# Kernel optimization log

Measured on AMD Instinct MI355X. Metric: run time of the kernel, lower is better.

## Reference

```python
import jax, jax.numpy as jnp
import numpy as np

B, S, D = 2, 512, 2048          # batch, seq, hidden
H, Dh = 16, 128                 # heads, head_dim
E, K, G, TG = 8, 2, 2, 1        # experts, top_k, n_group, topk_group
I, IS = 1024, 1024              # routed / shared expert intermediate
ROUTED_SCALE = 2.5
EPS = 1e-6
ROPE_THETA = 10000.0


def setup_inputs() -> dict:
    key = jax.random.key(0)
    ks = jax.random.split(key, 13)
    p = lambda k, shape, s=0.02: jax.random.normal(k, shape, jnp.float32) * s
    return {
        "hidden_states": jax.random.normal(ks[0], (B, S, D), jnp.float32),
        "ln1_w": jnp.ones((D,), jnp.float32),
        "ln2_w": jnp.ones((D,), jnp.float32),
        "wq": p(ks[1], (D, H * Dh)),
        "wk": p(ks[2], (D, H * Dh)),
        "wv": p(ks[3], (D, H * Dh)),
        "wo": p(ks[4], (H * Dh, D)),
        "gate_w": p(ks[5], (E, D)),
        "gate_bias": p(ks[6], (E,), 0.1),
        "w_gate": p(ks[7], (E, D, I)),
        "w_up": p(ks[8], (E, D, I)),
        "w_down": p(ks[9], (E, I, D)),
        "sw_gate": p(ks[10], (D, IS)),
        "sw_up": p(ks[11], (D, IS)),
        "sw_down": p(ks[12], (IS, D)),
    }


def _rmsnorm(x, w):
    var = jnp.mean(x * x, axis=-1, keepdims=True)
    return x * jax.lax.rsqrt(var + EPS) * w


def _rope_cos_sin(seq_len):
    inv_freq = 1.0 / (ROPE_THETA ** (jnp.arange(0, Dh, 2, dtype=jnp.float32) / Dh))
    ang = jnp.arange(seq_len, dtype=jnp.float32)[:, None] * inv_freq  # [S, Dh/2]
    return jnp.cos(ang)[None, :, None, :], jnp.sin(ang)[None, :, None, :]


def _apply_rope(x, cos, sin):
    x1, x2 = jnp.split(x, 2, axis=-1)
    return jnp.concatenate([x1 * cos - x2 * sin, x2 * cos + x1 * sin], axis=-1)


def _attention(x, wq, wk, wv, wo):
    q = (x @ wq).reshape(B, S, H, Dh)
    k = (x @ wk).reshape(B, S, H, Dh)
    v = (x @ wv).reshape(B, S, H, Dh)
    cos, sin = _rope_cos_sin(S)
    q = _apply_rope(q, cos, sin)
    k = _apply_rope(k, cos, sin)
    scores = jnp.einsum('bqhd,bkhd->bhqk', q, k) * (1.0 / np.sqrt(Dh).astype(np.float32))
    causal = jnp.tril(jnp.ones((S, S), bool))
    scores = jnp.where(causal, scores, jnp.finfo(scores.dtype).min)
    attn = jax.nn.softmax(scores, axis=-1)
    out = jnp.einsum('bhqk,bkhd->bqhd', attn, v).reshape(B, S, H * Dh)
    return out @ wo


def _moe(x, gate_w, gate_bias, w_gate, w_up, w_down, sw_gate, sw_up, sw_down):
    # x: [T, D]. noaux_tc grouped top-k routing (DeepSeek-V3 style).
    T = x.shape[0]
    logits = x @ gate_w.T                      # [T, E]
    scores = jax.nn.sigmoid(logits)
    sc = scores + gate_bias                    # selection scores with correction bias
    grp = sc.reshape(T, G, E // G)
    group_scores = jnp.sum(jax.lax.top_k(grp, 2)[0], axis=-1)  # top-2 sum per group [T,G]
    _, gidx = jax.lax.top_k(group_scores, TG)
    gmask = jnp.zeros((T, G), bool).at[jnp.arange(T)[:, None], gidx].set(True)
    emask = jnp.broadcast_to(gmask[:, :, None], (T, G, E // G)).reshape(T, E)
    masked = jnp.where(emask, sc, -jnp.inf)
    _, idx = jax.lax.top_k(masked, K)          # [T, K] expert ids
    w = jnp.take_along_axis(scores, idx, axis=-1)
    w = w / jnp.sum(w, axis=-1, keepdims=True)  # norm_topk_prob=True
    # dense combine weights [T, E] (zero except K entries per token)
    cw = jnp.zeros((T, E), x.dtype).at[jnp.arange(T)[:, None], idx].add(w)

    def body(acc, xs):
        wg, wu, wd, cwe = xs
        y = (jax.nn.silu(x @ wg) * (x @ wu)) @ wd  # SiluAndMul gated MLP
        return acc + cwe[:, None] * y, None

    routed, _ = jax.lax.scan(body, jnp.zeros_like(x), (w_gate, w_up, w_down, cw.T))
    shared = (jax.nn.silu(x @ sw_gate) * (x @ sw_up)) @ sw_down
    return routed * ROUTED_SCALE + shared


def reference(hidden_states, ln1_w, ln2_w, wq, wk, wv, wo, gate_w, gate_bias,
              w_gate, w_up, w_down, sw_gate, sw_up, sw_down):
    h = hidden_states
    h = h + _attention(_rmsnorm(h, ln1_w), wq, wk, wv, wo)
    x = _rmsnorm(h, ln2_w).reshape(B * S, D)
    moe_out = _moe(x, gate_w, gate_bias, w_gate, w_up, w_down,
                   sw_gate, sw_up, sw_down).reshape(B, S, D)
    return h + moe_out
```

## Files before the change

### kernel.cpp

```cpp
#include <hip/hip_runtime.h>

typedef __bf16 bf16x4 __attribute__((ext_vector_type(4)));
typedef __bf16 bf16x8 __attribute__((ext_vector_type(8)));
typedef _Float16 f16x4 __attribute__((ext_vector_type(4)));
typedef _Float16 f16x8 __attribute__((ext_vector_type(8)));
typedef float  f32x4  __attribute__((ext_vector_type(4)));

#define THREADS 256
constexpr int BK = 32, BKP = 40;

constexpr size_t MB = 1024*1024;
constexpr size_t oH2    = 0;
constexpr size_t oXB2   = 8*MB;
constexpr size_t oRT    = 12*MB;
constexpr size_t oWQKVT = 16*MB;
constexpr size_t oWOT   = 64*MB;
constexpr size_t oXN1   = 80*MB;
constexpr size_t oQKV   = 88*MB;
constexpr size_t oSCF   = 112*MB;
constexpr size_t oQKS   = 144*MB;
constexpr size_t oQKSL  = 152*MB;
constexpr size_t oVT    = 16*MB;
constexpr size_t oVTL   = 20*MB;
constexpr size_t oATT   = 24*MB;
constexpr size_t oPB    = 40*MB;
constexpr size_t oPBL2  = 88*MB;
constexpr size_t oWGUT  = 16*MB;
constexpr size_t oWDT   = 80*MB;
constexpr size_t oSGUT  = 112*MB;
constexpr size_t oSDT   = 120*MB;
constexpr size_t oHB    = 140*MB;
constexpr size_t oY     = 144*MB;
constexpr size_t oSHB   = 24*MB;
constexpr size_t oSDB   = 26*MB;
constexpr size_t oEIDX = oRT;
constexpr size_t oEW   = oRT + 8192;
constexpr size_t oSLOT = oRT + 16384;
constexpr size_t oLIST = oRT + 24576;
constexpr size_t oCNT  = oRT + 32768;
constexpr size_t oOFF  = oRT + 33024;
constexpr size_t oCUR  = oRT + 33280;

__device__ __forceinline__ bf16x8 bzero8() {
  bf16x8 z;
#pragma unroll
  for (int j = 0; j < 8; ++j) z[j] = (__bf16)0.f;
  return z;
}

template<int OM>
__global__ void transpose_kernel(const float* __restrict__ in, __bf16* __restrict__ out,
                                 int ldin, int ldout, int zlo,
                                 long inBH, long inBL, long outB, long plane) {
  __shared__ float tile[64][65];
  int z = blockIdx.z;
  const float* inp = in + (long)(z / zlo) * inBH + (long)(z % zlo) * inBL;
  __bf16* outp = out + (long)z * outB;
  int r0 = blockIdx.y * 64, c0 = blockIdx.x * 64;
  int tid = threadIdx.x;
#pragma unroll
  for (int i = 0; i < 4; ++i) {
    int lin = tid + i * 256;
    int r = lin >> 4, c4 = (lin & 15) << 2;
    f32x4 v = *(const f32x4*)(inp + (long)(r0 + r) * ldin + c0 + c4);
    tile[r][c4] = v[0]; tile[r][c4+1] = v[1]; tile[r][c4+2] = v[2]; tile[r][c4+3] = v[3];
  }
  __syncthreads();
#pragma unroll
  for (int i = 0; i < 4; ++i) {
    int lin = tid + i * 256;
    int oR = lin >> 4, oC4 = (lin & 15) << 2;
    __bf16* dst = outp + (long)(c0 + oR) * ldout + r0 + oC4;
    if constexpr (OM == 3) {
      f16x4 hv;
#pragma unroll
      for (int j = 0; j < 4; ++j) hv[j] = (_Float16)tile[oC4 + j][oR];
      *reinterpret_cast<f16x4*>(dst) = hv;
    } else {
      bf16x4 hi, lo;
#pragma unroll
      for (int j = 0; j < 4; ++j) {
        float v = tile[oC4 + j][oR];
        hi[j] = (__bf16)v;
        if constexpr (OM == 2) lo[j] = (__bf16)(v - (float)hi[j]);
      }
      *(bf16x4*)dst = hi;
      if constexpr (OM == 2) *(bf16x4*)(dst + plane) = lo;
    }
  }
}

template<int MODE, int SP, bool RESID, bool CAUSAL, bool KTRI, int TBM = 128, int TBN = 128>
__global__ __launch_bounds__(256, 2)
void gemm_kernel(const void* __restrict__ Av, const void* __restrict__ Bv, float* __restrict__ C,
                 const float* __restrict__ Rres,
                 int M, int N, int K, int lda, int ldb, int ldc,
                 int zlo, long aHi, long aLo, long bHi, long bLo, long cHi, long cLo,
                 long aPlane, long bPlane,
                 const int* __restrict__ counts, const int* __restrict__ offsets,
                 const int* __restrict__ gather) {
  const int n0 = blockIdx.x * TBN;
  const int m0 = blockIdx.y * TBM;
  const int z  = blockIdx.z;
  if (CAUSAL && n0 > m0) return;

  const float*  Af = (const float*)Av;
  const __bf16* Ah = (const __bf16*)Av;
  const __bf16* Bh = (const __bf16*)Bv;

  int mcount; int rowbase = 0;
  long aoff = 0, boff = 0, coff = 0;
  if constexpr (MODE == 0) {
    mcount = M;
    int zh = z / zlo, zl = z % zlo;
    aoff = (long)zh*aHi + (long)zl*aLo;
    boff = (long)zh*bHi + (long)zl*bLo;
    coff = (long)zh*cHi + (long)zl*cLo;
  } else {
    mcount = counts[z];
    rowbase = offsets[z];
    if (m0 >= mcount) return;
    boff = (long)z*bHi;
  }

  constexpr bool TRI  = (SP == 1 || SP == 2);
  constexpr bool F16  = (SP == 3 || SP == 4);
  constexpr bool AFLY = (SP == 1 || SP == 4);
  constexpr int ABUF = TBM*BKP;
  constexpr int BBUF = TBN*BKP;
  constexpr int WTM = TBM/2, WTN = TBN/2;
  constexpr int MI = WTM/16, MJ = WTN/16;
  __shared__ __align__(16) __bf16 As[(TRI?2:1)*ABUF];
  __shared__ __align__(16) __bf16 Bs[(TRI?2:1)*BBUF];

  const int tid = threadIdx.x;
  const int lane = tid & 63, wave = tid >> 6;
  const int wm = wave >> 1, wn = wave & 1;
  const int lq = lane >> 4, lr = lane & 15;

  int kend = K;
  if (KTRI) { int ke = m0 + TBM; kend = ke < K ? ke : K; }

  f32x4 acc[MI][MJ] = {};

  constexpr int NAF = AFLY ? TBM/32 : 1;
  constexpr int NAH = (!AFLY) ? TBM/64 : 1;
  constexpr int NB  = TBN/64;
  f32x4  arf[NAF];
  bf16x8 arh[NAH], arl[NAH];
  bf16x8 brh[NB],  brl[NB];

  auto loadAB = [&](int kk) {
    if constexpr (AFLY) {
#pragma unroll
      for (int it = 0; it < NAF; ++it) {
        int lin = tid + it*THREADS;
        int row = lin >> 3, c4 = (lin & 7) << 2;
        int gr = m0 + row;
        f32x4 zv; zv[0]=0.f; zv[1]=0.f; zv[2]=0.f; zv[3]=0.f;
        arf[it] = (gr < mcount) ? *(const f32x4*)(Af + aoff + (long)gr*lda + kk + c4) : zv;
      }
    } else {
#pragma unroll
      for (int it = 0; it < NAH; ++it) {
        int lin = tid + it*THREADS;
        int row = lin >> 2, c8 = (lin & 3) << 3;
        int gr = m0 + row;
        arh[it] = bzero8();
        if constexpr (SP == 2) arl[it] = bzero8();
        if (gr < mcount) {
          long arow;
          if constexpr (MODE == 1) arow = gather[rowbase + gr];
          else if constexpr (MODE == 2) arow = rowbase + gr;
          else arow = gr;
          const __bf16* p = Ah + aoff + arow*(long)lda + kk + c8;
          arh[it] = *(const bf16x8*)p;
          if constexpr (SP == 2) arl[it] = *(const bf16x8*)(p + aPlane);
        }
      }
    }
#pragma unroll
    for (int it = 0; it < NB; ++it) {
      int lin = tid + it*THREADS;
      int row = lin >> 2, c8 = (lin & 3) << 3;
      const __bf16* p = Bh + boff + (long)(n0+row)*ldb + kk + c8;
      brh[it] = *(const bf16x8*)p;
      if constexpr (TRI) brl[it] = *(const bf16x8*)(p + bPlane);
    }
  };

  auto writeAB = [&]() {
    if constexpr (AFLY) {
#pragma unroll
      for (int it = 0; it < NAF; ++it) {
        int lin = tid + it*THREADS;
        int row = lin >> 3, c4 = (lin & 7) << 2;
        if constexpr (SP == 4) {
          f16x4 hv;
#pragma unroll
          for (int j = 0; j < 4; ++j) hv[j] = (_Float16)arf[it][j];
          *reinterpret_cast<f16x4*>(As + row*BKP + c4) = hv;
        } else {
          bf16x4 hi, lo;
#pragma unroll
          for (int j = 0; j < 4; ++j) {
            hi[j] = (__bf16)arf[it][j];
            lo[j] = (__bf16)(arf[it][j] - (float)hi[j]);
          }
          *(bf16x4*)(As + row*BKP + c4) = hi;
          *(bf16x4*)(As + ABUF + row*BKP + c4) = lo;
        }
      }
    } else {
#pragma unroll
      for (int it = 0; it < NAH; ++it) {
        int lin = tid + it*THREADS;
        int row = lin >> 2, c8 = (lin & 3) << 3;
        *(bf16x8*)(As + row*BKP + c8) = arh[it];
        if constexpr (SP == 2) *(bf16x8*)(As + ABUF + row*BKP + c8) = arl[it];
      }
    }
#pragma unroll
    for (int it = 0; it < NB; ++it) {
      int lin = tid + it*THREADS;
      int row = lin >> 2, c8 = (lin & 3) << 3;
      *(bf16x8*)(Bs + row*BKP + c8) = brh[it];
      if constexpr (TRI) *(bf16x8*)(Bs + BBUF + row*BKP + c8) = brl[it];
    }
  };

  loadAB(0);
  writeAB();
  __syncthreads();

  for (int k0 = 0; k0 < kend; k0 += BK) {
    const bool hn = (k0 + BK < kend);
    if (hn) loadAB(k0 + BK);

    const __bf16* ap = As + (wm*WTM + lr)*BKP + lq*8;
    const __bf16* bp = Bs + (wn*WTN + lr)*BKP + lq*8;
    if constexpr (F16) {
      f16x8 fa[MI];
#pragma unroll
      for (int i = 0; i < MI; ++i)
        fa[i] = *reinterpret_cast<const f16x8*>(ap + i*16*BKP);
#pragma unroll
      for (int j = 0; j < MJ; ++j) {
        f16x8 fb = *reinterpret_cast<const f16x8*>(bp + j*16*BKP);
#pragma unroll
        for (int i = 0; i < MI; ++i)
          acc[i][j] = __builtin_amdgcn_mfma_f32_16x16x32_f16(fa[i], fb, acc[i][j], 0, 0, 0);
      }
    } else {
      bf16x8 fa[MI], fal[MI];
#pragma unroll
      for (int i = 0; i < MI; ++i) {
        fa[i] = *(const bf16x8*)(ap + i*16*BKP);
        if constexpr (TRI) fal[i] = *(const bf16x8*)(ap + ABUF + i*16*BKP);
      }
#pragma unroll
      for (int j = 0; j < MJ; ++j) {
        bf16x8 fb = *(const bf16x8*)(bp + j*16*BKP);
        if constexpr (TRI) {
          bf16x8 fbl = *(const bf16x8*)(bp + BBUF + j*16*BKP);
#pragma unroll
          for (int i = 0; i < MI; ++i) {
            acc[i][j] = __builtin_amdgcn_mfma_f32_16x16x32_bf16(fa[i],  fbl, acc[i][j], 0, 0, 0);
            acc[i][j] = __builtin_amdgcn_mfma_f32_16x16x32_bf16(fal[i], fb,  acc[i][j], 0, 0, 0);
            acc[i][j] = __builtin_amdgcn_mfma_f32_16x16x32_bf16(fa[i],  fb,  acc[i][j], 0, 0, 0);
          }
        } else {
#pragma unroll
          for (int i = 0; i < MI; ++i)
            acc[i][j] = __builtin_amdgcn_mfma_f32_16x16x32_bf16(fa[i], fb, acc[i][j], 0, 0, 0);
        }
      }
    }

    if (hn) {
      __syncthreads();
      writeAB();
      __syncthreads();
    }
  }

#pragma unroll
  for (int i = 0; i < MI; ++i) {
#pragma unroll
    for (int rg = 0; rg < 4; ++rg) {
      int lrow = wm*WTM + i*16 + lq*4 + rg;
      int gr = m0 + lrow;
      if (gr < mcount) {
        long crow = coff + (long)(rowbase + gr)*ldc;
#pragma unroll
        for (int j = 0; j < MJ; ++j) {
          int col = n0 + wn*WTN + j*16 + lr;
          float val = acc[i][j][rg];
          if constexpr (RESID) val += Rres[(long)gr*ldc + col];
          C[crow + col] = val;
        }
      }
    }
  }
}

template<int MODE>
__global__ __launch_bounds__(256, 2)
void gugemm_kernel(const __bf16* __restrict__ A, const __bf16* __restrict__ B,
                   __bf16* __restrict__ O, int M, int K, int lda, int ldb, long bHi,
                   const int* __restrict__ counts, const int* __restrict__ offsets,
                   const int* __restrict__ gather) {
  const int n0 = blockIdx.x * 64;
  const int m0 = blockIdx.y * 64;
  const int z  = blockIdx.z;

  int mcount; int rowbase = 0; long boff = 0;
  if constexpr (MODE == 1) {
    mcount = counts[z];
    rowbase = offsets[z];
    if (m0 >= mcount) return;
    boff = (long)z*bHi;
  } else {
    mcount = M;
  }

  constexpr int TBUF = 64*BKP;
  __shared__ __align__(16) __bf16 As[TBUF];
  __shared__ __align__(16) __bf16 Bg[TBUF];
  __shared__ __align__(16) __bf16 Bu[TBUF];

  const int tid = threadIdx.x;
  const int lane = tid & 63, wave = tid >> 6;
  const int wm = wave >> 1, wn = wave & 1;
  const int lq = lane >> 4, lr = lane & 15;

  f32x4 accG[2][2] = {}, accU[2][2] = {};

  bf16x8 ar, bg, bu;
  const int srow = tid >> 2, sc8 = (tid & 3) << 3;
  long aBase; bool aOK;
  {
    int gr = m0 + srow;
    aOK = gr < mcount;
    long arow = 0;
    if (aOK) {
      if constexpr (MODE == 1) arow = gather[rowbase + gr];
      else arow = gr;
    }
    aBase = arow*(long)lda;
  }
  const long gBase = boff + (long)(n0 + srow)*ldb;
  const long uBase = boff + (long)(1024 + n0 + srow)*ldb;

  auto loadAB = [&](int kk) {
    ar = aOK ? *(const bf16x8*)(A + aBase + kk + sc8) : bzero8();
    bg = *(const bf16x8*)(B + gBase + kk + sc8);
    bu = *(const bf16x8*)(B + uBase + kk + sc8);
  };
  auto writeAB = [&]() {
    *(bf16x8*)(As + srow*BKP + sc8) = ar;
    *(bf16x8*)(Bg + srow*BKP + sc8) = bg;
    *(bf16x8*)(Bu + srow*BKP + sc8) = bu;
  };

  loadAB(0);
  writeAB();
  __syncthreads();

  for (int k0 = 0; k0 < K; k0 += BK) {
    const bool hn = (k0 + BK < K);
    if (hn) loadAB(k0 + BK);

    const __bf16* ap  = As + (wm*32 + lr)*BKP + lq*8;
    const __bf16* bgp = Bg + (wn*32 + lr)*BKP + lq*8;
    const __bf16* bup = Bu + (wn*32 + lr)*BKP + lq*8;
    bf16x8 fa[2];
    fa[0] = *(const bf16x8*)(ap);
    fa[1] = *(const bf16x8*)(ap + 16*BKP);
#pragma unroll
    for (int j = 0; j < 2; ++j) {
      bf16x8 fg = *(const bf16x8*)(bgp + j*16*BKP);
      bf16x8 fu = *(const bf16x8*)(bup + j*16*BKP);
#pragma unroll
      for (int i = 0; i < 2; ++i) {
        accG[i][j] = __builtin_amdgcn_mfma_f32_16x16x32_bf16(fa[i], fg, accG[i][j], 0, 0, 0);
        accU[i][j] = __builtin_amdgcn_mfma_f32_16x16x32_bf16(fa[i], fu, accU[i][j], 0, 0, 0);
      }
    }

    if (hn) {
      __syncthreads();
      writeAB();
      __syncthreads();
    }
  }

#pragma unroll
  for (int i = 0; i < 2; ++i) {
#pragma unroll
    for (int rg = 0; rg < 4; ++rg) {
      int lrow = wm*32 + i*16 + lq*4 + rg;
      int gr = m0 + lrow;
      if (gr < mcount) {
        long orow = (long)(rowbase + gr)*1024;
#pragma unroll
        for (int j = 0; j < 2; ++j) {
          int col = n0 + wn*32 + j*16 + lr;
          float g = accG[i][j][rg], u = accU[i][j][rg];
          float val = (g / (1.f + expf(-g))) * u;
          O[orow + col] = (__bf16)val;
        }
      }
    }
  }
}

template<int OM>
__global__ void rmsnorm_kernel(const float* __restrict__ x, const float* __restrict__ w,
                               __bf16* __restrict__ out, long plane) {
  const int row = blockIdx.x;
  const float* xr = x + (long)row * 2048;
  float ss = 0.f;
  for (int d = threadIdx.x; d < 2048; d += 256) { float v = xr[d]; ss += v*v; }
  __shared__ float red[4];
  int lane = threadIdx.x & 63, wave = threadIdx.x >> 6;
#pragma unroll
  for (int off = 32; off; off >>= 1) ss += __shfl_down(ss, off, 64);
  if (lane == 0) red[wave] = ss;
  __syncthreads();
  float tot = red[0] + red[1] + red[2] + red[3];
  float rs = rsqrtf(tot * (1.f/2048.f) + 1e-6f);
  __bf16* orow = out + (long)row * 2048;
  for (int d = threadIdx.x; d < 2048; d += 256) {
    float v = xr[d]*rs*w[d];
    if constexpr (OM == 3) {
      ((_Float16*)orow)[d] = (_Float16)v;
    } else {
      __bf16 h = (__bf16)v;
      orow[d] = h;
      if constexpr (OM == 2) orow[d + plane] = (__bf16)(v - (float)h);
    }
  }
}

__global__ void rope_split_kernel(const float* __restrict__ qkv, __bf16* __restrict__ o, long plane) {
  int tid = blockIdx.x*256 + threadIdx.x;
  int i = tid & 63;
  int th = tid >> 6;
  int h = th & 15;
  int t = th >> 4;
  int s = t & 511;
  long ib = (long)t*6144 + h*128;
  long ob = (long)t*4096 + h*128;
  float inv = 1.f / powf(10000.f, (float)i * (1.f/64.f));
  float ang = (float)s * inv;
  float c = cosf(ang), sn = sinf(ang);
  float q1 = qkv[ib+i], q2 = qkv[ib+64+i];
  float r1 = q1*c - q2*sn, r2 = q2*c + q1*sn;
  __bf16 h1 = (__bf16)r1, h2v = (__bf16)r2;
  o[ob+i] = h1;            o[ob+i+plane] = (__bf16)(r1 - (float)h1);
  o[ob+64+i] = h2v;        o[ob+64+i+plane] = (__bf16)(r2 - (float)h2v);
  float k1 = qkv[ib+2048+i], k2 = qkv[ib+2048+64+i];
  float s1 = k1*c - k2*sn, s2 = k2*c + k1*sn;
  __bf16 g1 = (__bf16)s1, g2 = (__bf16)s2;
  o[ob+2048+i] = g1;       o[ob+2048+i+plane] = (__bf16)(s1 - (float)g1);
  o[ob+2048+64+i] = g2;    o[ob+2048+64+i+plane] = (__bf16)(s2 - (float)g2);
}

__global__ void softmax_kernel(const float* __restrict__ sc, __bf16* __restrict__ p, long plane) {
  int r = blockIdx.x & 511;
  long bh = blockIdx.x >> 9;
  const float scale = 0.08838834764831845f;
  long base = (bh*512 + r)*512;
  int c0 = threadIdx.x, c1 = threadIdx.x + 256;
  float v0 = (c0 <= r) ? sc[base+c0]*scale : -3.0e38f;
  float v1 = (c1 <= r) ? sc[base+c1]*scale : -3.0e38f;
  float m = fmaxf(v0, v1);
  __shared__ float red[4];
  int lane = threadIdx.x & 63, wave = threadIdx.x >> 6;
#pragma unroll
  for (int off = 32; off; off >>= 1) m = fmaxf(m, __shfl_xor(m, off, 64));
  if (lane == 0) red[wave] = m;
  __syncthreads();
  m = fmaxf(fmaxf(red[0], red[1]), fmaxf(red[2], red[3]));
  __syncthreads();
  float e0 = (c0 <= r) ? expf(v0 - m) : 0.f;
  float e1 = (c1 <= r) ? expf(v1 - m) : 0.f;
  float s = e0 + e1;
#pragma unroll
  for (int off = 32; off; off >>= 1) s += __shfl_xor(s, off, 64);
  if (lane == 0) red[wave] = s;
  __syncthreads();
  s = red[0] + red[1] + red[2] + red[3];
  float inv = 1.f / s;
  float p0 = e0*inv, p1 = e1*inv;
  __bf16 h0 = (__bf16)p0, h1 = (__bf16)p1;
  p[base+c0] = h0; p[base+c0+plane] = (__bf16)(p0 - (float)h0);
  p[base+c1] = h1; p[base+c1+plane] = (__bf16)(p1 - (float)h1);
}

__global__ void zero8_kernel(int* c) { if (threadIdx.x < 8) c[threadIdx.x] = 0; }

__global__ void routing_kernel(const float* __restrict__ h2, const float* __restrict__ ln2w,
                               const float* __restrict__ gw, const float* __restrict__ gb,
                               __bf16* __restrict__ xb2,
                               int* __restrict__ eidx, float* __restrict__ ew,
                               int* __restrict__ counts) {
  int t = blockIdx.x;
  const float* xr = h2 + (long)t*2048;
  int lane = threadIdx.x & 63, wave = threadIdx.x >> 6;
  float ss = 0.f;
  for (int d = threadIdx.x; d < 2048; d += 256) { float v = xr[d]; ss += v*v; }
  __shared__ float red[4];
#pragma unroll
  for (int off = 32; off; off >>= 1) ss += __shfl_down(ss, off, 64);
  if (lane == 0) red[wave] = ss;
  __syncthreads();
  float rs = rsqrtf((red[0]+red[1]+red[2]+red[3]) * (1.f/2048.f) + 1e-6f);
  __bf16* xrow = xb2 + (long)t*2048;
  for (int d = threadIdx.x; d < 2048; d += 256) xrow[d] = (__bf16)(xr[d]*rs*ln2w[d]);
  __shared__ float lg[8];
  for (int e = wave; e < 8; e += 4) {
    const float* wr = gw + (long)e*2048;
    float acc = 0.f;
    for (int d = lane; d < 2048; d += 64) acc += (xr[d]*rs*ln2w[d]) * wr[d];
#pragma unroll
    for (int off = 32; off; off >>= 1) acc += __shfl_down(acc, off, 64);
    if (lane == 0) lg[e] = acc;
  }
  __syncthreads();
  if (threadIdx.x == 0) {
    float sg[8], sc[8];
#pragma unroll
    for (int e = 0; e < 8; ++e) { sg[e] = 1.f/(1.f+expf(-lg[e])); sc[e] = sg[e] + gb[e]; }
    float gs[2];
#pragma unroll
    for (int g = 0; g < 2; ++g) {
      float m1 = -3e38f, m2 = -3e38f;
#pragma unroll
      for (int j = 0; j < 4; ++j) {
        float v = sc[4*g+j];
        if (v > m1) { m2 = m1; m1 = v; } else if (v > m2) m2 = v;
      }
      gs[g] = m1 + m2;
    }
    int b4 = (gs[1] > gs[0]) ? 4 : 0;
    int i1 = 0; float v1 = -3e38f;
#pragma unroll
    for (int j = 0; j < 4; ++j) if (sc[b4+j] > v1) { v1 = sc[b4+j]; i1 = j; }
    int i2 = -1; float v2 = -3e38f;
#pragma unroll
    for (int j = 0; j < 4; ++j) if (j != i1 && sc[b4+j] > v2) { v2 = sc[b4+j]; i2 = j; }
    float w1 = sg[b4+i1], w2 = sg[b4+i2], s = w1 + w2;
    eidx[t*2] = b4+i1; eidx[t*2+1] = b4+i2;
    ew[t*2] = w1/s;    ew[t*2+1] = w2/s;
    atomicAdd(&counts[b4+i1], 1); atomicAdd(&counts[b4+i2], 1);
  }
}

__global__ void scan_kernel(const int* __restrict__ counts, int* __restrict__ offsets,
                            int* __restrict__ cursors) {
  if (threadIdx.x == 0 && blockIdx.x == 0) {
    int s = 0;
    for (int e = 0; e < 8; ++e) { offsets[e] = s; s += counts[e]; cursors[e] = 0; }
    offsets[8] = s;
  }
}

__global__ void scatter_kernel(const int* __restrict__ eidx, const int* __restrict__ offsets,
                               int* __restrict__ cursors, int* __restrict__ list,
                               int* __restrict__ slot) {
  int t = blockIdx.x*256 + threadIdx.x;
  if (t < 1024) {
#pragma unroll
    for (int kk = 0; kk < 2; ++kk) {
      int e = eidx[t*2+kk];
      int pos = atomicAdd(&cursors[e], 1);
      int g = offsets[e] + pos;
      list[g] = t;
      slot[t*2+kk] = g;
    }
  }
}

__global__ void combine_kernel(const float* __restrict__ h2, const float* __restrict__ y,
                               const float* __restrict__ sdown, const int* __restrict__ slot,
                               const float* __restrict__ ew, float* __restrict__ out) {
  int i = blockIdx.x*256 + threadIdx.x;
  int t = i >> 11;
  int d = i & 2047;
  float rv = ew[t*2]   * y[(long)slot[t*2]  *2048 + d]
           + ew[t*2+1] * y[(long)slot[t*2+1]*2048 + d];
  out[i] = h2[i] + sdown[i] + 2.5f * rv;
}

extern "C" void kernel_launch(void* const* d_in, const int* in_sizes, int n_in,
                              void* d_out, int out_size, void* d_ws, size_t ws_size,
                              hipStream_t stream) {
  const float* hid  = (const float*)d_in[0];
  const float* ln1  = (const float*)d_in[1];
  const float* ln2  = (const float*)d_in[2];
  const float* wq   = (const float*)d_in[3];
  const float* wk   = (const float*)d_in[4];
  const float* wv   = (const float*)d_in[5];
  const float* wo   = (const float*)d_in[6];
  const float* gw   = (const float*)d_in[7];
  const float* gb   = (const float*)d_in[8];
  const float* wgat = (const float*)d_in[9];
  const float* wup  = (const float*)d_in[10];
  const float* wdn  = (const float*)d_in[11];
  const float* swg  = (const float*)d_in[12];
  const float* swu  = (const float*)d_in[13];
  const float* swd  = (const float*)d_in[14];
  float* out = (float*)d_out;
  char* ws = (char*)d_ws;

  float*  h2    = (float*)(ws + oH2);
  __bf16* xb2   = (__bf16*)(ws + oXB2);
  __bf16* wqkvT = (__bf16*)(ws + oWQKVT);
  __bf16* woT   = (__bf16*)(ws + oWOT);
  __bf16* xn1   = (__bf16*)(ws + oXN1);
  float*  qkv   = (float*)(ws + oQKV);
  float*  scf   = (float*)(ws + oSCF);
  __bf16* qks   = (__bf16*)(ws + oQKS);
  __bf16* vtb   = (__bf16*)(ws + oVT);
  float*  att   = (float*)(ws + oATT);
  __bf16* pb    = (__bf16*)(ws + oPB);
  __bf16* wgut  = (__bf16*)(ws + oWGUT);
  __bf16* wdt   = (__bf16*)(ws + oWDT);
  __bf16* sgut  = (__bf16*)(ws + oSGUT);
  __bf16* sdt   = (__bf16*)(ws + oSDT);
  __bf16* hb    = (__bf16*)(ws + oHB);
  float*  ybuf  = (float*)(ws + oY);
  __bf16* shb   = (__bf16*)(ws + oSHB);
  float*  sdb   = (float*)(ws + oSDB);
  int*   eidx = (int*)(ws + oEIDX);
  float* ew   = (float*)(ws + oEW);
  int*   slot = (int*)(ws + oSLOT);
  int*   list = (int*)(ws + oLIST);
  int*   cnt  = (int*)(ws + oCNT);
  int*   offs = (int*)(ws + oOFF);
  int*   curs = (int*)(ws + oCUR);

  const long S22 = (long)2048*2048, S21 = (long)2048*1024;
  const long pQKS  = (oQKSL - oQKS) / 2;
  const long pVT   = 2*MB;
  const long pPB   = (oPBL2 - oPB) / 2;

  transpose_kernel<3><<<dim3(32,32,1), 256, 0, stream>>>(wq, wqkvT,          2048, 2048, 1, 0, 0, 0, 0);
  transpose_kernel<3><<<dim3(32,32,1), 256, 0, stream>>>(wk, wqkvT + S22,    2048, 2048, 1, 0, 0, 0, 0);
  transpose_kernel<3><<<dim3(32,32,1), 256, 0, stream>>>(wv, wqkvT + 2*S22,  2048, 2048, 1, 0, 0, 0, 0);
  transpose_kernel<3><<<dim3(32,32,1), 256, 0, stream>>>(wo, woT,            2048, 2048, 1, 0, 0, 0, 0);

  rmsnorm_kernel<3><<<1024, 256, 0, stream>>>(hid, ln1, xn1, 0);

  gemm_kernel<0, 3, false, false, false, 64, 128><<<dim3(48,16,1), 256, 0, stream>>>(
      xn1, wqkvT, qkv, nullptr, 1024, 6144, 2048, 2048, 2048, 6144,
      1, 0, 0, 0, 0, 0, 0, 0, 0, nullptr, nullptr, nullptr);

  rope_split_kernel<<<4096, 256, 0, stream>>>(qkv, qks, pQKS);

  transpose_kernel<2><<<dim3(2,8,32), 256, 0, stream>>>(
      qkv + 4096, vtb, 6144, 512, 16, (long)512*6144, 128, (long)128*512, pVT);

  gemm_kernel<0, 2, false, true, false, 64, 64><<<dim3(8,8,32), 256, 0, stream>>>(
      qks, qks + 2048, scf, nullptr, 512, 512, 128, 4096, 4096, 512,
      16, (long)512*4096, 128, (long)512*4096, 128, (long)16*512*512, (long)512*512,
      pQKS, pQKS, nullptr, nullptr, nullptr);

  softmax_kernel<<<16384, 256, 0, stream>>>(scf, pb, pPB);

  gemm_kernel<0, 2, false, false, true, 64, 64><<<dim3(2,8,32), 256, 0, stream>>>(
      pb, vtb, att, nullptr, 512, 128, 512, 512, 512, 2048,
      16, (long)16*512*512, (long)512*512, (long)16*128*512, (long)128*512,
      (long)512*2048, 128, pPB, pVT, nullptr, nullptr, nullptr);

  gemm_kernel<0, 4, true, false, false, 64, 64><<<dim3(32,16,1), 256, 0, stream>>>(
      att, woT, h2, hid, 1024, 2048, 2048, 2048, 2048, 2048,
      1, 0, 0, 0, 0, 0, 0, 0, 0, nullptr, nullptr, nullptr);

  zero8_kernel<<<1, 64, 0, stream>>>(cnt);
  routing_kernel<<<1024, 256, 0, stream>>>(h2, ln2, gw, gb, xb2, eidx, ew, cnt);
  scan_kernel<<<1, 64, 0, stream>>>(cnt, offs, curs);
  scatter_kernel<<<4, 256, 0, stream>>>(eidx, offs, curs, list, slot);

  transpose_kernel<1><<<dim3(16,32,8), 256, 0, stream>>>(wgat, wgut,        1024, 2048, 1, S21, 0, S22, 0);
  transpose_kernel<1><<<dim3(16,32,8), 256, 0, stream>>>(wup,  wgut + S21,  1024, 2048, 1, S21, 0, S22, 0);
  transpose_kernel<1><<<dim3(32,16,8), 256, 0, stream>>>(wdn,  wdt,         2048, 1024, 1, S21, 0, S21, 0);
  transpose_kernel<1><<<dim3(16,32,1), 256, 0, stream>>>(swg,  sgut,        1024, 2048, 1, 0, 0, 0, 0);
  transpose_kernel<1><<<dim3(16,32,1), 256, 0, stream>>>(swu,  sgut + S21,  1024, 2048, 1, 0, 0, 0, 0);
  transpose_kernel<1><<<dim3(32,16,1), 256, 0, stream>>>(swd,  sdt,         2048, 1024, 1, 0, 0, 0, 0);

  gugemm_kernel<1><<<dim3(16,16,8), 256, 0, stream>>>(
      xb2, wgut, hb, 1024, 2048, 2048, 2048, S22, cnt, offs, list);
  gemm_kernel<2, 0, false, false, false, 64, 64><<<dim3(32,16,8), 256, 0, stream>>>(
      hb, wdt, ybuf, nullptr, 1024, 2048, 1024, 1024, 1024, 2048,
      1, 0, 0, S21, 0, 0, 0, 0, 0, cnt, offs, nullptr);

  gugemm_kernel<0><<<dim3(16,16,1), 256, 0, stream>>>(
      xb2, sgut, shb, 1024, 2048, 2048, 2048, 0, nullptr, nullptr, nullptr);
  gemm_kernel<0, 0, false, false, false, 64, 64><<<dim3(32,16,1), 256, 0, stream>>>(
      shb, sdt, sdb, nullptr, 1024, 2048, 1024, 1024, 1024, 2048,
      1, 0, 0, 0, 0, 0, 0, 0, 0, nullptr, nullptr, nullptr);

  combine_kernel<<<8192, 256, 0, stream>>>(h2, ybuf, sdb, slot, ew, out);
}
```

Baseline: 706.1 us.

## Merge shared expert into grouped MoE GEMMs as ninth expert, widen gugemm K tile

The shared expert becomes a ninth group (z=8) in the grouped gate/up and down GEMM launches. Its weights are laid out contiguously after the routed experts, and counts[8]=1024 is set in the scan kernel. This removes two separate kernel launches and lets the shared-expert work fill the same grid as the routed experts. The gate/up kernel also moves from a K tile of 32 to 64, with two rows per thread per load, halving the number of barrier pairs per K sweep at the cost of more shared memory and registers. The combine kernel reads the shared output from rows 2048+ of the joint output buffer.

```diff
diff --git a/kernel.cpp b/kernel.cpp
--- a/kernel.cpp
+++ b/kernel.cpp
@@ -26,13 +26,11 @@
 constexpr size_t oPB    = 40*MB;
 constexpr size_t oPBL2  = 88*MB;
 constexpr size_t oWGUT  = 16*MB;
-constexpr size_t oWDT   = 80*MB;
-constexpr size_t oSGUT  = 112*MB;
+constexpr size_t oSGUT  = 80*MB;
+constexpr size_t oWDT   = 88*MB;
 constexpr size_t oSDT   = 120*MB;
-constexpr size_t oHB    = 140*MB;
-constexpr size_t oY     = 144*MB;
-constexpr size_t oSHB   = 24*MB;
-constexpr size_t oSDB   = 26*MB;
+constexpr size_t oHBC   = 124*MB;
+constexpr size_t oYC    = 130*MB;
 constexpr size_t oEIDX = oRT;
 constexpr size_t oEW   = oRT + 8192;
 constexpr size_t oSLOT = oRT + 16384;
@@ -304,27 +302,23 @@
   }
 }
 
-template<int MODE>
 __global__ __launch_bounds__(256, 2)
 void gugemm_kernel(const __bf16* __restrict__ A, const __bf16* __restrict__ B,
-                   __bf16* __restrict__ O, int M, int K, int lda, int ldb, long bHi,
+                   __bf16* __restrict__ O, int K, int lda, int ldb, long bHi,
                    const int* __restrict__ counts, const int* __restrict__ offsets,
                    const int* __restrict__ gather) {
+  constexpr int BKg = 64, BKP2 = 72;
   const int n0 = blockIdx.x * 64;
   const int m0 = blockIdx.y * 64;
   const int z  = blockIdx.z;
 
-  int mcount; int rowbase = 0; long boff = 0;
-  if constexpr (MODE == 1) {
-    mcount = counts[z];
-    rowbase = offsets[z];
-    if (m0 >= mcount) return;
-    boff = (long)z*bHi;
-  } else {
-    mcount = M;
-  }
-
-  constexpr int TBUF = 64*BKP;
+  const int mcount = counts[z];
+  const int rowbase = offsets[z];
+  if (m0 >= mcount) return;
+  const long boff = (long)z*bHi;
+  const bool shared = (z == 8);
+
+  constexpr int TBUF = 64*BKP2;
   __shared__ __align__(16) __bf16 As[TBUF];
   __shared__ __align__(16) __bf16 Bg[TBUF];
   __shared__ __align__(16) __bf16 Bu[TBUF];
@@ -336,55 +330,65 @@
 
   f32x4 accG[2][2] = {}, accU[2][2] = {};
 
-  bf16x8 ar, bg, bu;
-  const int srow = tid >> 2, sc8 = (tid & 3) << 3;
-  long aBase; bool aOK;
+  const int r0 = tid >> 3;
+  const int c8 = (tid & 7) << 3;
+  long aB0, aB1; bool aOK0, aOK1;
   {
-    int gr = m0 + srow;
-    aOK = gr < mcount;
-    long arow = 0;
-    if (aOK) {
-      if constexpr (MODE == 1) arow = gather[rowbase + gr];
-      else arow = gr;
-    }
-    aBase = arow*(long)lda;
-  }
-  const long gBase = boff + (long)(n0 + srow)*ldb;
-  const long uBase = boff + (long)(1024 + n0 + srow)*ldb;
-
+    int g0 = m0 + r0, g1 = m0 + r0 + 32;
+    aOK0 = g0 < mcount; aOK1 = g1 < mcount;
+    long ar0 = 0, ar1 = 0;
+    if (aOK0) ar0 = shared ? g0 : gather[rowbase + g0];
+    if (aOK1) ar1 = shared ? g1 : gather[rowbase + g1];
+    aB0 = ar0*(long)lda; aB1 = ar1*(long)lda;
+  }
+  const long gB0 = boff + (long)(n0 + r0)*ldb;
+  const long gB1 = boff + (long)(n0 + r0 + 32)*ldb;
+  const long uB0 = boff + (long)(1024 + n0 + r0)*ldb;
+  const long uB1 = boff + (long)(1024 + n0 + r0 + 32)*ldb;
+
+  bf16x8 ar0v, ar1v, bg0, bg1, bu0, bu1;
   auto loadAB = [&](int kk) {
-    ar = aOK ? *(const bf16x8*)(A + aBase + kk + sc8) : bzero8();
-    bg = *(const bf16x8*)(B + gBase + kk + sc8);
-    bu = *(const bf16x8*)(B + uBase + kk + sc8);
+    ar0v = aOK0 ? *(const bf16x8*)(A + aB0 + kk + c8) : bzero8();
+    ar1v = aOK1 ? *(const bf16x8*)(A + aB1 + kk + c8) : bzero8();
+    bg0 = *(const bf16x8*)(B + gB0 + kk + c8);
+    bg1 = *(const bf16x8*)(B + gB1 + kk + c8);
+    bu0 = *(const bf16x8*)(B + uB0 + kk + c8);
+    bu1 = *(const bf16x8*)(B + uB1 + kk + c8);
   };
   auto writeAB = [&]() {
-    *(bf16x8*)(As + srow*BKP + sc8) = ar;
-    *(bf16x8*)(Bg + srow*BKP + sc8) = bg;
-    *(bf16x8*)(Bu + srow*BKP + sc8) = bu;
+    *(bf16x8*)(As + r0*BKP2 + c8) = ar0v;
+    *(bf16x8*)(As + (r0+32)*BKP2 + c8) = ar1v;
+    *(bf16x8*)(Bg + r0*BKP2 + c8) = bg0;
+    *(bf16x8*)(Bg + (r0+32)*BKP2 + c8) = bg1;
+    *(bf16x8*)(Bu + r0*BKP2 + c8) = bu0;
+    *(bf16x8*)(Bu + (r0+32)*BKP2 + c8) = bu1;
   };
 
   loadAB(0);
   writeAB();
   __syncthreads();
 
-  for (int k0 = 0; k0 < K; k0 += BK) {
-    const bool hn = (k0 + BK < K);
-    if (hn) loadAB(k0 + BK);
-
-    const __bf16* ap  = As + (wm*32 + lr)*BKP + lq*8;
-    const __bf16* bgp = Bg + (wn*32 + lr)*BKP + lq*8;
-    const __bf16* bup = Bu + (wn*32 + lr)*BKP + lq*8;
-    bf16x8 fa[2];
-    fa[0] = *(const bf16x8*)(ap);
-    fa[1] = *(const bf16x8*)(ap + 16*BKP);
-#pragma unroll
-    for (int j = 0; j < 2; ++j) {
-      bf16x8 fg = *(const bf16x8*)(bgp + j*16*BKP);
-      bf16x8 fu = *(const bf16x8*)(bup + j*16*BKP);
-#pragma unroll
-      for (int i = 0; i < 2; ++i) {
-        accG[i][j] = __builtin_amdgcn_mfma_f32_16x16x32_bf16(fa[i], fg, accG[i][j], 0, 0, 0);
-        accU[i][j] = __builtin_amdgcn_mfma_f32_16x16x32_bf16(fa[i], fu, accU[i][j], 0, 0, 0);
+  for (int k0 = 0; k0 < K; k0 += BKg) {
+    const bool hn = (k0 + BKg < K);
+    if (hn) loadAB(k0 + BKg);
+
+    const __bf16* ap  = As + (wm*32 + lr)*BKP2 + lq*8;
+    const __bf16* bgp = Bg + (wn*32 + lr)*BKP2 + lq*8;
+    const __bf16* bup = Bu + (wn*32 + lr)*BKP2 + lq*8;
+#pragma unroll
+    for (int ks = 0; ks < BKg; ks += 32) {
+      bf16x8 fa[2];
+      fa[0] = *(const bf16x8*)(ap + ks);
+      fa[1] = *(const bf16x8*)(ap + 16*BKP2 + ks);
+#pragma unroll
+      for (int j = 0; j < 2; ++j) {
+        bf16x8 fg = *(const bf16x8*)(bgp + j*16*BKP2 + ks);
+        bf16x8 fu = *(const bf16x8*)(bup + j*16*BKP2 + ks);
+#pragma unroll
+        for (int i = 0; i < 2; ++i) {
+          accG[i][j] = __builtin_amdgcn_mfma_f32_16x16x32_bf16(fa[i], fg, accG[i][j], 0, 0, 0);
+          accU[i][j] = __builtin_amdgcn_mfma_f32_16x16x32_bf16(fa[i], fu, accU[i][j], 0, 0, 0);
+        }
       }
     }
 
@@ -558,12 +562,13 @@
   }
 }
 
-__global__ void scan_kernel(const int* __restrict__ counts, int* __restrict__ offsets,
-                            int* __restrict__ cursors) {
+__global__ void scan_kernel(const int* __restrict__ counts_in, int* __restrict__ counts,
+                            int* __restrict__ offsets, int* __restrict__ cursors) {
   if (threadIdx.x == 0 && blockIdx.x == 0) {
     int s = 0;
     for (int e = 0; e < 8; ++e) { offsets[e] = s; s += counts[e]; cursors[e] = 0; }
     offsets[8] = s;
+    counts[8]  = 1024;
   }
 }
 
@@ -584,14 +589,15 @@
 }
 
 __global__ void combine_kernel(const float* __restrict__ h2, const float* __restrict__ y,
-                               const float* __restrict__ sdown, const int* __restrict__ slot,
+                               const int* __restrict__ slot,
                                const float* __restrict__ ew, float* __restrict__ out) {
   int i = blockIdx.x*256 + threadIdx.x;
   int t = i >> 11;
   int d = i & 2047;
   float rv = ew[t*2]   * y[(long)slot[t*2]  *2048 + d]
            + ew[t*2+1] * y[(long)slot[t*2+1]*2048 + d];
-  out[i] = h2[i] + sdown[i] + 2.5f * rv;
+  float sh = y[(long)(2048 + t)*2048 + d];
+  out[i] = h2[i] + sh + 2.5f * rv;
 }
 
 extern "C" void kernel_launch(void* const* d_in, const int* in_sizes, int n_in,
@@ -627,13 +633,11 @@
   float*  att   = (float*)(ws + oATT);
   __bf16* pb    = (__bf16*)(ws + oPB);
   __bf16* wgut  = (__bf16*)(ws + oWGUT);
+  __bf16* sgut  = (__bf16*)(ws + oSGUT);
   __bf16* wdt   = (__bf16*)(ws + oWDT);
-  __bf16* sgut  = (__bf16*)(ws + oSGUT);
   __bf16* sdt   = (__bf16*)(ws + oSDT);
-  __bf16* hb    = (__bf16*)(ws + oHB);
-  float*  ybuf  = (float*)(ws + oY);
-  __bf16* shb   = (__bf16*)(ws + oSHB);
-  float*  sdb   = (float*)(ws + oSDB);
+  __bf16* hbc   = (__bf16*)(ws + oHBC);
+  float*  ybc   = (float*)(ws + oYC);
   int*   eidx = (int*)(ws + oEIDX);
   float* ew   = (float*)(ws + oEW);
   int*   slot = (int*)(ws + oSLOT);
@@ -681,7 +685,7 @@
 
   zero8_kernel<<<1, 64, 0, stream>>>(cnt);
   routing_kernel<<<1024, 256, 0, stream>>>(h2, ln2, gw, gb, xb2, eidx, ew, cnt);
-  scan_kernel<<<1, 64, 0, stream>>>(cnt, offs, curs);
+  scan_kernel<<<1, 64, 0, stream>>>(cnt, cnt, offs, curs);
   scatter_kernel<<<4, 256, 0, stream>>>(eidx, offs, curs, list, slot);
 
   transpose_kernel<1><<<dim3(16,32,8), 256, 0, stream>>>(wgat, wgut,        1024, 2048, 1, S21, 0, S22, 0);
@@ -691,17 +695,11 @@
   transpose_kernel<1><<<dim3(16,32,1), 256, 0, stream>>>(swu,  sgut + S21,  1024, 2048, 1, 0, 0, 0, 0);
   transpose_kernel<1><<<dim3(32,16,1), 256, 0, stream>>>(swd,  sdt,         2048, 1024, 1, 0, 0, 0, 0);
 
-  gugemm_kernel<1><<<dim3(16,16,8), 256, 0, stream>>>(
-      xb2, wgut, hb, 1024, 2048, 2048, 2048, S22, cnt, offs, list);
-  gemm_kernel<2, 0, false, false, false, 64, 64><<<dim3(32,16,8), 256, 0, stream>>>(
-      hb, wdt, ybuf, nullptr, 1024, 2048, 1024, 1024, 1024, 2048,
+  gugemm_kernel<<<dim3(16,16,9), 256, 0, stream>>>(
+      xb2, wgut, hbc, 2048, 2048, 2048, S22, cnt, offs, list);
+  gemm_kernel<2, 0, false, false, false, 64, 64><<<dim3(32,16,9), 256, 0, stream>>>(
+      hbc, wdt, ybc, nullptr, 1024, 2048, 1024, 1024, 1024, 2048,
       1, 0, 0, S21, 0, 0, 0, 0, 0, cnt, offs, nullptr);
 
-  gugemm_kernel<0><<<dim3(16,16,1), 256, 0, stream>>>(
-      xb2, sgut, shb, 1024, 2048, 2048, 2048, 0, nullptr, nullptr, nullptr);
-  gemm_kernel<0, 0, false, false, false, 64, 64><<<dim3(32,16,1), 256, 0, stream>>>(
-      shb, sdt, sdb, nullptr, 1024, 2048, 1024, 1024, 1024, 2048,
-      1, 0, 0, 0, 0, 0, 0, 0, 0, nullptr, nullptr, nullptr);
-
-  combine_kernel<<<8192, 256, 0, stream>>>(h2, ybuf, sdb, slot, ew, out);
-}
+  combine_kernel<<<8192, 256, 0, stream>>>(h2, ybc, slot, ew, out);
+}
```

New measurement: 650.7 us. -7.8%, faster.
